# Optimization experiments

Hardware: AMD Instinct MI355X
Metric: run time of the kernel (lower is better)

## Reference

```python
import jax, jax.numpy as jnp
import numpy as np


def setup_inputs() -> dict:
    key = jax.random.key(0)
    k1, k2, k3 = jax.random.split(key, 3)
    B, D, F, P = 4096, 1024, 2048, 1024
    return {
        "x": jax.random.normal(k1, (B, D), dtype=jnp.float32),
        "features": jax.random.normal(k2, (F, D), dtype=jnp.float32),
        "prototypes": jax.random.normal(k3, (P, D), dtype=jnp.float32),
        "alpha": jnp.ones((1,), dtype=jnp.float32),
        "beta": jnp.ones((1,), dtype=jnp.float32),
        "theta": jnp.ones((1,), dtype=jnp.float32),
    }


def reference(x, features, prototypes, alpha, beta, theta):
    # Project each set ONCE (the original redundantly broadcasts first).
    xf = x @ features.T            # [B, F]
    pf = prototypes @ features.T   # [P, F]
    sx = jax.nn.sigmoid(xf)        # x_present [B, F]
    sp = jax.nn.sigmoid(pf)        # p_present [P, F]
    ax = xf * sx                   # [B, F]
    bp = pf * sp                   # [P, F]
    # common[b,p]        = sum_f xf*pf*sx*sp            = (xf*sx) @ (pf*sp)^T
    # x_distinct[b,p]    = sum_f xf*sx*(1-sp)           = rowsum(xf*sx) - (xf*sx) @ sp^T
    # p_distinct[b,p]    = sum_f pf*sp*(1-sx)           = rowsum(pf*sp) - sx @ (pf*sp)^T
    common = ax @ bp.T                                     # [B, P]
    x_distinctive = ax.sum(axis=1, keepdims=True) - ax @ sp.T  # [B, P]
    p_distinctive = bp.sum(axis=1)[None, :] - sx @ bp.T        # [B, P]
    return theta * common - alpha * x_distinctive - beta * p_distinctive
```

## Files before the change

kernel.cpp:

```cpp
#include <hip/hip_runtime.h>
#include <hip/hip_bf16.h>

typedef __bf16 bf16_t;
typedef bf16_t bf16x4 __attribute__((ext_vector_type(4)));
typedef bf16_t bf16x8 __attribute__((ext_vector_type(8)));
typedef float f32x4 __attribute__((ext_vector_type(4)));

#define AS1 __attribute__((address_space(1)))
#define AS3 __attribute__((address_space(3)))

__device__ __forceinline__ void gload_lds16(const void* g, void* l) {
    __builtin_amdgcn_global_load_lds((const AS1 void*)g, (AS3 void*)l, 16, 0, 0);
}
__device__ __forceinline__ void gload_lds4(const void* g, void* l) {
    __builtin_amdgcn_global_load_lds((const AS1 void*)g, (AS3 void*)l, 4, 0, 0);
}

__device__ __forceinline__ float sigmoidf_(float v) {
    return 1.0f / (1.0f + __expf(-v));
}

__global__ __launch_bounds__(256) void k_convert3(const float* __restrict__ x,
                                                  const float* __restrict__ pr,
                                                  const float* __restrict__ ft,
                                                  bf16_t* __restrict__ XPs,
                                                  bf16_t* __restrict__ F16s) {
    const int n4 = 7168 * 256;
    int i = blockIdx.x * 256 + threadIdx.x;
    const int stride = gridDim.x * 256;
    for (; i < n4; i += stride) {
        float4 v;
        long r;
        int c4;
        bf16_t* dst;
        long R;
        if (i < 1048576) {
            v = ((const float4*)x)[i];
            r = i >> 8; c4 = i & 255; dst = XPs; R = 5120;
        } else if (i < 1310720) {
            const int j = i - 1048576;
            v = ((const float4*)pr)[j];
            r = 4096 + (j >> 8); c4 = j & 255; dst = XPs; R = 5120;
        } else {
            const int j = i - 1310720;
            v = ((const float4*)ft)[j];
            r = j >> 8; c4 = j & 255; dst = F16s; R = 2048;
        }
        const int col = c4 << 2;
        const int kb = col >> 5;
        const int cw = col & 31;
        bf16x4 o;
        o[0] = (bf16_t)v.x; o[1] = (bf16_t)v.y; o[2] = (bf16_t)v.z; o[3] = (bf16_t)v.w;
        *(bf16x4*)(dst + ((long)kb * R + r) * 32 + cw) = o;
    }
}

__global__ __launch_bounds__(256) void k_reduce4(const bf16_t* __restrict__ part,
                                                 const float* __restrict__ rsPart,
                                                 const float* __restrict__ pa,
                                                 float* __restrict__ out) {
    const int blk = blockIdx.x;
    const int t = threadIdx.x;
    const int idx = blk * 256 + t;
    const int region = idx >> 13;
    const int widx = idx & 8191;
    const int wv = widx >> 10;
    const int chunk = (widx >> 6) & 15;
    const int ln = widx & 63;
    const int bx = region >> 2, by = region & 3;
    const int wm = wv >> 2, wn = wv & 3;
    const int fg = chunk >> 1, gp = chunk & 1;
    const int er = (ln >> 4) << 2, ec = ln & 15;
    const long off = (long)idx * 8;
    const int c = blk & 31;

    __shared__ float rowsum[32];
    __shared__ float colsum[64];
    const int base_r = bx * 256 + wm * 128 + (c & 3) * 32;
    const int base_c = by * 256 + wn * 64;
    if (t < 32) {
        float s = 0.f;
#pragma unroll
        for (int b = 0; b < 8; ++b) s += rsPart[b * 5120 + base_r + t];
        rowsum[t] = pa[0] * s;
    } else if (t < 96) {
        const int cc = t - 32;
        float s = 0.f;
#pragma unroll
        for (int b = 0; b < 8; ++b) s += rsPart[b * 5120 + 4096 + base_c + cc];
        colsum[cc] = s;
    }

    float sum[8] = {};
#pragma unroll
    for (int s = 0; s < 4; ++s) {
        bf16x8 v = *(const bf16x8*)(part + (long)s * 4194304 + off);
#pragma unroll
        for (int j = 0; j < 8; ++j) sum[j] += (float)v[j];
    }
    __syncthreads();

    const int r0 = bx * 256 + wm * 128 + fg * 16 + er;
    const int c0 = by * 256 + wn * 64 + gp * 32 + ec;
#pragma unroll
    for (int q = 0; q < 4; ++q) {
        const float ra = rowsum[r0 + q - base_r];
#pragma unroll
        for (int gh = 0; gh < 2; ++gh) {
            const int col = c0 + gh * 16;
            out[(long)(r0 + q) * 1024 + col] = sum[gh * 4 + q] - ra - colsum[col - base_c];
        }
    }
}

__global__ __launch_bounds__(512, 2) void gemm2_8p(
    const char* __restrict__ A8, const char* __restrict__ B8,
    bf16_t* __restrict__ O1, long zstride) {
    __shared__ char lds[65536];
    const int tid = threadIdx.x;
    const int wave = tid >> 6, lane = tid & 63;
    const int wm = wave >> 2, wn = wave & 3;
    const int lm = lane & 15;

    const int gx = gridDim.x, gy = gridDim.y;
    const int o = blockIdx.x + gx * (blockIdx.y + gy * blockIdx.z);
    const int cpx = (gx * gy * (int)gridDim.z) >> 3;
    const int v = (o & 7) * cpx + (o >> 3);
    const int bx = v % gx;
    const int rem = v / gx;
    const int by = rem % gy;
    const int bz = rem / gy;

    const long bm = (long)bx * 256, bn = (long)by * 256;
    const int kb32_0 = bz * 32;

    const int base_a = (lane >> 4) * 2048 + (wm * 128 + lm) * 8;
    const int base_b = (lane >> 4) * 2048 + (wn * 64 + lm) * 8;

    f32x4 acc[8][4] = {};

#define VM4 asm volatile("s_waitcnt vmcnt(4)" ::: "memory")
#define VM2 asm volatile("s_waitcnt vmcnt(2)" ::: "memory")
#define VM0 asm volatile("s_waitcnt vmcnt(0)" ::: "memory")

    auto PFETCH = [&](int pf) {
        const long kb = kb32_0 + pf;
        const int ps = pf & 3;
        const int kg = tid >> 7;
        const int li = (tid & 127) << 4;
        gload_lds16(A8 + kb * 131072 + (long)kg * 32768 + bm * 8 + li,
                    lds + ps * 8192 + wave * 1024);
        gload_lds16(B8 + kb * 32768 + (long)kg * 8192 + bn * 8 + li,
                    lds + 32768 + ps * 8192 + wave * 1024);
    };

#define PHASE2(p, WAITSTMT, DOPF)                                               \
    do {                                                                        \
        WAITSTMT;                                                               \
        __builtin_amdgcn_s_barrier();                                           \
        __builtin_amdgcn_s_setprio(1);                                          \
        const int slot = (p) & 3;                                               \
        const char* sA = lds + slot * 8192;                                     \
        const char* sB = lds + 32768 + slot * 8192;                             \
        long long af[8];                                                        \
        long long bfr[4];                                                       \
        _Pragma("unroll") for (int f = 0; f < 8; ++f)                           \
            af[f] = *(const long long*)(sA + base_a + f * 128);                 \
        _Pragma("unroll") for (int g = 0; g < 4; ++g)                           \
            bfr[g] = *(const long long*)(sB + base_b + g * 128);                \
        if (DOPF) PFETCH((p) + 3);                                              \
        _Pragma("unroll") for (int f = 0; f < 8; ++f)                           \
            _Pragma("unroll") for (int g = 0; g < 4; ++g)                       \
                acc[f][g] = __builtin_amdgcn_mfma_f32_16x16x32_fp8_fp8(         \
                    af[f], bfr[g], acc[f][g], 0, 0, 0);                         \
        __builtin_amdgcn_s_setprio(0);                                          \
    } while (0)

    const int NP = 32;
    PFETCH(0);
    PFETCH(1);
    PFETCH(2);

    for (int p = 0; p < NP - 3; ++p) PHASE2(p, VM4, 1);
    PHASE2(NP - 3, VM4, 0);
    PHASE2(NP - 2, VM2, 0);
    PHASE2(NP - 1, VM0, 0);

#undef PHASE2
#undef VM4
#undef VM2
#undef VM0

    bf16_t* Op = O1 + (long)bz * zstride + (long)(bx * 4 + by) * 65536 +
                 wave * 8192 + lane * 8;
#pragma unroll
    for (int fg = 0; fg < 8; ++fg)
#pragma unroll
        for (int gp = 0; gp < 2; ++gp) {
            bf16x8 w;
#pragma unroll
            for (int gh = 0; gh < 2; ++gh)
#pragma unroll
                for (int q = 0; q < 4; ++q)
                    w[gh * 4 + q] = (bf16_t)acc[fg][gp * 2 + gh][q];
            *(bf16x8*)(Op + (fg * 2 + gp) * 512) = w;
        }
}

__global__ __launch_bounds__(512, 2) void gemm1_160(
    const bf16_t* __restrict__ XPs, const bf16_t* __restrict__ F16s,
    char* __restrict__ A8, char* __restrict__ B8,
    float* __restrict__ rsPart,
    const float* __restrict__ pa, const float* __restrict__ pb,
    const float* __restrict__ pt) {
    __shared__ char lds[106496];
    const int tid = threadIdx.x;
    const int wave = tid >> 6, lane = tid & 63;
    const int wm = wave >> 2, wn = wave & 3;

    const int gx = gridDim.x, gy = gridDim.y;
    const int o = blockIdx.x + gx * blockIdx.y;
    const int cpx = (gx * gy) >> 3;
    const int v = (o & 7) * cpx + (o >> 3);
    const int bx = v % gx;
    const int by = v / gx;

    const long bm = (long)bx * 160, bn = (long)by * 256;
    const char* Ab = (const char*)XPs;
    const char* Bb = (const char*)F16s;

    const int swzcb = ((lane >> 4) << 4) ^ (((lane >> 3) & 1) << 5);
    const int base_a = (wm * 80 + (lane & 15)) * 64 + swzcb;
    const int base_b = (wn * 64 + (lane & 15)) * 64 + swzcb;

    f32x4 acc[5][4] = {};

#define VM8 asm volatile("s_waitcnt vmcnt(8)" ::: "memory")
#define VM4 asm volatile("s_waitcnt vmcnt(4)" ::: "memory")
#define VM0 asm volatile("s_waitcnt vmcnt(0)" ::: "memory")

    auto PFETCH = [&](int pf) {
        const int ps = pf & 3;
        const char* Ag = Ab + ((long)pf * 5120 + bm) * 64;
        const char* Bg = Bb + ((long)pf * 2048 + bn) * 64;
        {
            const int oo = tid << 4;
            const int cb = (oo & 63) ^ (((oo >> 9) & 1) << 5);
            gload_lds16(Ag + (oo & ~63) + cb, lds + ps * 10240 + (oo & ~1023));
        }
        {
            const int oo = 8192 + (tid << 2);
            const int cb = (oo & 63) ^ (((oo >> 9) & 1) << 5);
            gload_lds4(Ag + (oo & ~63) + cb, lds + ps * 10240 + 8192 + wave * 256);
        }
#pragma unroll
        for (int j = 0; j < 2; ++j) {
            const int oo = (j * 512 + tid) << 4;
            const int cb = (oo & 63) ^ (((oo >> 9) & 1) << 5);
            gload_lds16(Bg + (oo & ~63) + cb, lds + 40960 + ps * 16384 + (oo & ~1023));
        }
    };

#define PHASE1(p, WAITSTMT, DOPF)                                               \
    do {                                                                        \
        WAITSTMT;                                                               \
        __builtin_amdgcn_s_barrier();                                           \
        __builtin_amdgcn_s_setprio(1);                                          \
        const int slot = (p) & 3;                                               \
        const char* sA = lds + slot * 10240;                                    \
        const char* sB = lds + 40960 + slot * 16384;                            \
        bf16x8 af[5];                                                           \
        bf16x8 bfr[4];                                                          \
        _Pragma("unroll") for (int f = 0; f < 5; ++f)                           \
            af[f] = *(const bf16x8*)(sA + base_a + f * 1024);                   \
        _Pragma("unroll") for (int g = 0; g < 4; ++g)                           \
            bfr[g] = *(const bf16x8*)(sB + base_b + g * 1024);                  \
        if (DOPF) PFETCH((p) + 3);                                              \
        _Pragma("unroll") for (int f = 0; f < 5; ++f)                           \
            _Pragma("unroll") for (int g = 0; g < 4; ++g)                       \
                acc[f][g] = __builtin_amdgcn_mfma_f32_16x16x32_bf16(            \
                    bfr[g], af[f], acc[f][g], 0, 0, 0);                         \
        __builtin_amdgcn_s_setprio(0);                                          \
    } while (0)

    const int NP = 32;
    PFETCH(0);
    PFETCH(1);
    PFETCH(2);

    for (int p = 0; p < NP - 3; ++p) PHASE1(p, VM8, 1);
    PHASE1(NP - 3, VM8, 0);
    PHASE1(NP - 2, VM4, 0);
    PHASE1(NP - 1, VM0, 0);

#undef PHASE1
#undef VM8
#undef VM4
#undef VM0

    const float va = pa[0], vb = pb[0], vt = pt[0];
    const int lm = lane & 15;
    const int ln4 = (lane >> 4) << 2;
    const int kbbase = (int)(bn >> 5) + wn * 2;
    float rs[5];
#pragma unroll
    for (int f = 0; f < 5; ++f) rs[f] = 0.f;

#pragma unroll
    for (int mf = 0; mf < 5; ++mf) {
        const long grow = bm + wm * 80 + mf * 16 + lm;
        const bool isXf = (grow < 4096);
        const long rowidx = isXf ? grow : (grow - 4096);
        const long rowsz = isXf ? 4096 : 1024;
        char* base = isXf ? A8 : B8;
#pragma unroll
        for (int g = 0; g < 4; ++g) {
            float o0[4], o1[4];
            float rsl = 0.f;
#pragma unroll
            for (int q = 0; q < 4; ++q) {
                const float vv = acc[mf][g][q];
                const float s = sigmoidf_(vv);
                const float prod = vv * s;
                o0[q] = isXf ? prod : (vt * prod + va * s);
                o1[q] = isXf ? s : (vb * prod);
                rsl += isXf ? prod : vb * prod;
            }
            rs[mf] += rsl;
            int u0 = __builtin_amdgcn_cvt_pk_fp8_f32(o0[0], o0[1], 0, false);
            u0 = __builtin_amdgcn_cvt_pk_fp8_f32(o0[2], o0[3], u0, true);
            int u1 = __builtin_amdgcn_cvt_pk_fp8_f32(o1[0], o1[1], 0, false);
            u1 = __builtin_amdgcn_cvt_pk_fp8_f32(o1[2], o1[3], u1, true);
            const long kb = kbbase + (g >> 1);
            const int fbase = (g & 1) * 16 + ln4;
            const int kgrp = fbase >> 3;
            const int sub = fbase & 7;
            *(int*)(base + ((kb * 4 + kgrp) * rowsz + rowidx) * 8 + sub) = u0;
            *(int*)(base + (((kb + 64) * 4 + kgrp) * rowsz + rowidx) * 8 + sub) = u1;
        }
    }

    __syncthreads();
    float* lds_f = (float*)lds;
#pragma unroll
    for (int f = 0; f < 5; ++f) {
        float t = rs[f];
        t += __shfl_xor(t, 16);
        t += __shfl_xor(t, 32);
        if ((lane >> 4) == 0) lds_f[wn * 160 + wm * 80 + f * 16 + lm] = t;
    }
    __syncthreads();
    if (tid < 160) {
        const float s = lds_f[tid] + lds_f[160 + tid] + lds_f[320 + tid] + lds_f[480 + tid];
        rsPart[(long)by * 5120 + bm + tid] = s;
    }
}

extern "C" void kernel_launch(void* const* d_in, const int* in_sizes, int n_in,
                              void* d_out, int out_size, void* d_ws, size_t ws_size,
                              hipStream_t stream) {
    const float* x = (const float*)d_in[0];
    const float* feats = (const float*)d_in[1];
    const float* protos = (const float*)d_in[2];
    const float* pa = (const float*)d_in[3];
    const float* pb = (const float*)d_in[4];
    const float* pt = (const float*)d_in[5];
    float* out = (float*)d_out;

    constexpr long Bsz = 4096, D = 1024, F = 2048, P = 1024;

    bf16_t* XPs = (bf16_t*)d_ws;
    bf16_t* F16s = XPs + (Bsz + P) * D;
    char* A8 = (char*)(F16s + F * D);
    char* B8 = A8 + 128L * 4 * 4096 * 8;
    float* rsPart = (float*)(B8 + 128L * 4 * 1024 * 8);
    bf16_t* part = (bf16_t*)(rsPart + 8 * 5120);

    k_convert3<<<2048, 256, 0, stream>>>(x, protos, feats, XPs, F16s);

    gemm1_160<<<dim3(32, 8), 512, 0, stream>>>(XPs, F16s, A8, B8, rsPart, pa, pb, pt);

    gemm2_8p<<<dim3(Bsz / 256, P / 256, 4), 512, 0, stream>>>(
        A8, B8, part, (long)Bsz * P);

    k_reduce4<<<2048, 256, 0, stream>>>(part, rsPart, pa, out);
}
```

Measured before the change: 79.19 us.

## Fuse split-K reduction into gemm2 via last-block atomic counter

Removes the separate reduce kernel. Each gemm2 block writes its bf16 split-K partial, then bumps a per-tile atomic counter. The last block to arrive for a tile sums the other partials with its own register accumulators, subtracts the row and column sums, and writes the output. This drops one kernel launch and the re-read of its own partial. In exchange it adds a memset, fences and atomics, and puts a serial tail on the last-arriving blocks.

New measurement: 169.5 us. 2.14x slower.

```diff
diff --git a/kernel.cpp b/kernel.cpp
--- a/kernel.cpp
+++ b/kernel.cpp
@@ -55,67 +55,11 @@
     }
 }
 
-__global__ __launch_bounds__(256) void k_reduce4(const bf16_t* __restrict__ part,
-                                                 const float* __restrict__ rsPart,
-                                                 const float* __restrict__ pa,
-                                                 float* __restrict__ out) {
-    const int blk = blockIdx.x;
-    const int t = threadIdx.x;
-    const int idx = blk * 256 + t;
-    const int region = idx >> 13;
-    const int widx = idx & 8191;
-    const int wv = widx >> 10;
-    const int chunk = (widx >> 6) & 15;
-    const int ln = widx & 63;
-    const int bx = region >> 2, by = region & 3;
-    const int wm = wv >> 2, wn = wv & 3;
-    const int fg = chunk >> 1, gp = chunk & 1;
-    const int er = (ln >> 4) << 2, ec = ln & 15;
-    const long off = (long)idx * 8;
-    const int c = blk & 31;
-
-    __shared__ float rowsum[32];
-    __shared__ float colsum[64];
-    const int base_r = bx * 256 + wm * 128 + (c & 3) * 32;
-    const int base_c = by * 256 + wn * 64;
-    if (t < 32) {
-        float s = 0.f;
-#pragma unroll
-        for (int b = 0; b < 8; ++b) s += rsPart[b * 5120 + base_r + t];
-        rowsum[t] = pa[0] * s;
-    } else if (t < 96) {
-        const int cc = t - 32;
-        float s = 0.f;
-#pragma unroll
-        for (int b = 0; b < 8; ++b) s += rsPart[b * 5120 + 4096 + base_c + cc];
-        colsum[cc] = s;
-    }
-
-    float sum[8] = {};
-#pragma unroll
-    for (int s = 0; s < 4; ++s) {
-        bf16x8 v = *(const bf16x8*)(part + (long)s * 4194304 + off);
-#pragma unroll
-        for (int j = 0; j < 8; ++j) sum[j] += (float)v[j];
-    }
-    __syncthreads();
-
-    const int r0 = bx * 256 + wm * 128 + fg * 16 + er;
-    const int c0 = by * 256 + wn * 64 + gp * 32 + ec;
-#pragma unroll
-    for (int q = 0; q < 4; ++q) {
-        const float ra = rowsum[r0 + q - base_r];
-#pragma unroll
-        for (int gh = 0; gh < 2; ++gh) {
-            const int col = c0 + gh * 16;
-            out[(long)(r0 + q) * 1024 + col] = sum[gh * 4 + q] - ra - colsum[col - base_c];
-        }
-    }
-}
-
 __global__ __launch_bounds__(512, 2) void gemm2_8p(
     const char* __restrict__ A8, const char* __restrict__ B8,
-    bf16_t* __restrict__ O1, long zstride) {
+    bf16_t* __restrict__ O1, long zstride,
+    const float* __restrict__ rsPart, const float* __restrict__ pa,
+    float* __restrict__ out, int* __restrict__ cnt) {
     __shared__ char lds[65536];
     const int tid = threadIdx.x;
     const int wave = tid >> 6, lane = tid & 63;
@@ -191,8 +135,8 @@
 #undef VM2
 #undef VM0
 
-    bf16_t* Op = O1 + (long)bz * zstride + (long)(bx * 4 + by) * 65536 +
-                 wave * 8192 + lane * 8;
+    const int tile = bx * 4 + by;
+    bf16_t* Op = O1 + (long)bz * zstride + (long)tile * 65536 + wave * 8192 + lane * 8;
 #pragma unroll
     for (int fg = 0; fg < 8; ++fg)
 #pragma unroll
@@ -204,6 +148,63 @@
                 for (int q = 0; q < 4; ++q)
                     w[gh * 4 + q] = (bf16_t)acc[fg][gp * 2 + gh][q];
             *(bf16x8*)(Op + (fg * 2 + gp) * 512) = w;
+        }
+
+    __threadfence();
+    __shared__ int lastFlag;
+    if (tid == 0) lastFlag = (atomicAdd(&cnt[tile], 1) == 3);
+    __syncthreads();
+    if (!lastFlag) return;
+    __threadfence();
+
+    float* rowsum = (float*)lds;
+    float* colsum = rowsum + 256;
+    if (tid < 256) {
+        float s = 0.f;
+#pragma unroll
+        for (int b = 0; b < 8; ++b) s += rsPart[b * 5120 + bm + tid];
+        rowsum[tid] = pa[0] * s;
+    } else {
+        const int cc = tid - 256;
+        float s = 0.f;
+#pragma unroll
+        for (int b = 0; b < 8; ++b) s += rsPart[b * 5120 + 4096 + bn + cc];
+        colsum[cc] = s;
+    }
+    __syncthreads();
+
+    const bf16_t* Pbase = O1 + (long)tile * 65536 + wave * 8192 + lane * 8;
+    const int er = (lane >> 4) << 2;
+    const int ec = lane & 15;
+#pragma unroll
+    for (int fg = 0; fg < 8; ++fg)
+#pragma unroll
+        for (int gp = 0; gp < 2; ++gp) {
+            float sum[8] = {};
+            const long coff = (fg * 2 + gp) * 512;
+            for (int z = 0; z < 4; ++z) {
+                if (z == bz) {
+#pragma unroll
+                    for (int gh = 0; gh < 2; ++gh)
+#pragma unroll
+                        for (int q = 0; q < 4; ++q)
+                            sum[gh * 4 + q] += (float)(bf16_t)acc[fg][gp * 2 + gh][q];
+                } else {
+                    bf16x8 vv = *(const bf16x8*)(Pbase + (long)z * zstride + coff);
+#pragma unroll
+                    for (int j = 0; j < 8; ++j) sum[j] += (float)vv[j];
+                }
+            }
+#pragma unroll
+            for (int gh = 0; gh < 2; ++gh) {
+                const int lc = wn * 64 + (gp * 2 + gh) * 16 + ec;
+                const float cs = colsum[lc];
+#pragma unroll
+                for (int q = 0; q < 4; ++q) {
+                    const int lr = wm * 128 + fg * 16 + er + q;
+                    out[(bm + lr) * 1024 + bn + lc] = sum[gh * 4 + q] - rowsum[lr] - cs;
+                }
+            }
         }
 }
 
@@ -375,13 +376,14 @@
     char* B8 = A8 + 128L * 4 * 4096 * 8;
     float* rsPart = (float*)(B8 + 128L * 4 * 1024 * 8);
     bf16_t* part = (bf16_t*)(rsPart + 8 * 5120);
+    int* cnt = (int*)(part + 4L * Bsz * P);
+
+    hipMemsetAsync(cnt, 0, 64 * sizeof(int), stream);
 
     k_convert3<<<2048, 256, 0, stream>>>(x, protos, feats, XPs, F16s);
 
     gemm1_160<<<dim3(32, 8), 512, 0, stream>>>(XPs, F16s, A8, B8, rsPart, pa, pb, pt);
 
     gemm2_8p<<<dim3(Bsz / 256, P / 256, 4), 512, 0, stream>>>(
-        A8, B8, part, (long)Bsz * P);
-
-    k_reduce4<<<2048, 256, 0, stream>>>(part, rsPart, pa, out);
-}
+        A8, B8, part, (long)Bsz * P, rsPart, pa, out, cnt);
+}
```
